# Kernel optimization log

Hardware: AMD Instinct MI355X
Metric: run time of the kernel (lower is better)

## Reference

```python
import jax, jax.numpy as jnp
import numpy as np
import math

B, SQ, SKV, D = 16, 1024, 1024, 256


def setup_inputs() -> dict:
    key = jax.random.key(0)
    kq, kk, kv, km = jax.random.split(key, 4)
    # Scale inputs down: the module applies exp() to raw QK^T logits, so dot
    # products must stay small to avoid overflow (std ~ 0.05^2*sqrt(D) ~ 0.04).
    scale = 0.05
    query = jax.random.normal(kq, (B, SQ, D), dtype=jnp.float32) * scale
    key_t = jax.random.normal(kk, (B, SKV, D), dtype=jnp.float32) * scale
    value = jax.random.normal(kv, (B, SKV, D), dtype=jnp.float32)
    mask = jax.random.randint(km, (B, SQ, SKV), 0, 2, dtype=jnp.int32)
    return {"query": query, "key": key_t, "value": value, "mask": mask}


def reference(query, key, value, mask):
    # scores = exp(Q K^T) / sqrt(d)  -- note: exp BEFORE scaling, as in source
    d = query.shape[-1]
    inv_sqrt_d = jnp.float32(1.0 / math.sqrt(d))
    scores = jnp.exp(jnp.einsum('bqd,bkd->bqk', query, key)) * inv_sqrt_d
    # masked_fill(mask == 0, -1e9)
    scores = jnp.where(mask == 0, jnp.float32(-1e9), scores)
    p_attn = jax.nn.softmax(scores, axis=-1)
    # dropout is identity in eval mode (deterministic reference)
    output = jnp.einsum('bqk,bkd->bqd', p_attn, value)
    # flatten=True path: sum over the query/sequence dim
    return output.sum(axis=1), p_attn
```

## Files before the change

### kernel.cpp

```cpp
#include <hip/hip_runtime.h>

#define NB   16
#define NSQ  1024
#define NSKV 1024
#define ND   256

typedef __bf16    bf16x8 __attribute__((ext_vector_type(8)));
typedef float     f32x4  __attribute__((ext_vector_type(4)));
typedef _Float16  f16x4  __attribute__((ext_vector_type(4)));

#define KST 264

__global__ __launch_bounds__(256) void cvt_k_bf16(
    const float* __restrict__ src, __bf16* __restrict__ dst)
{
    const int i = blockIdx.x * 256 + threadIdx.x;
    const float4* s = (const float4*)src + (size_t)i * 2;
    float4 a = s[0], b = s[1];
    bf16x8 o;
    o[0] = (__bf16)a.x; o[1] = (__bf16)a.y; o[2] = (__bf16)a.z; o[3] = (__bf16)a.w;
    o[4] = (__bf16)b.x; o[5] = (__bf16)b.y; o[6] = (__bf16)b.z; o[7] = (__bf16)b.w;
    ((bf16x8*)dst)[i] = o;
}

__global__ __launch_bounds__(256) void pack_mask(
    const int* __restrict__ mask, unsigned* __restrict__ mw)
{
    const int row = blockIdx.x * 4 + (threadIdx.x >> 6);
    const int l   = threadIdx.x & 63;
    const int4* mrow = (const int4*)(mask + (size_t)row * NSKV) + l * 4;
    unsigned w = 0;
    #pragma unroll
    for (int v = 0; v < 4; ++v) {
        int4 mv = mrow[v];
        w |= (mv.x != 0 ? 1u : 0u) << (v * 4 + 0);
        w |= (mv.y != 0 ? 1u : 0u) << (v * 4 + 1);
        w |= (mv.z != 0 ? 1u : 0u) << (v * 4 + 2);
        w |= (mv.w != 0 ? 1u : 0u) << (v * 4 + 3);
    }
    const int m    = l & 15;
    const int base = l & 48;
    unsigned out = 0;
    #pragma unroll
    for (int c = 0; c < 16; ++c) {
        unsigned v = (unsigned)__shfl((int)w, base | c);
        out |= ((v >> m) & 1u) << c;
    }
    mw[(size_t)row * 64 + l] = out;
}

__global__ __launch_bounds__(256, 2) void attn_fused(
    const float* __restrict__ Q, const __bf16* __restrict__ Kb,
    const unsigned* __restrict__ mw, float* __restrict__ out_p,
    float* __restrict__ colsum)
{
    const int b    = blockIdx.x >> 6;
    const int qt   = blockIdx.x & 63;
    const int q0   = qt * 16;
    const int tid  = threadIdx.x;
    const int lane = tid & 63;
    const int h    = tid >> 6;
    const int m    = lane & 15;
    const int kg   = lane >> 4;

    __shared__ __attribute__((aligned(16))) __bf16 kbuf[4][2][16 * KST];
    __shared__ float Zs[4][16];
    __shared__ float invZs[16];

    bf16x8 afrag[8];
    {
        const float* qbase = Q + ((size_t)(b * NSQ + q0 + m)) * ND;
        #pragma unroll
        for (int dc = 0; dc < 8; ++dc) {
            const float* p4 = qbase + dc * 32 + kg * 8;
            float4 x = *(const float4*)(p4);
            float4 y = *(const float4*)(p4 + 4);
            bf16x8 a;
            a[0] = (__bf16)x.x; a[1] = (__bf16)x.y; a[2] = (__bf16)x.z; a[3] = (__bf16)x.w;
            a[4] = (__bf16)y.x; a[5] = (__bf16)y.y; a[6] = (__bf16)y.z; a[7] = (__bf16)y.w;
            afrag[dc] = a;
        }
    }

    unsigned mword[4];
    #pragma unroll
    for (int i = 0; i < 4; ++i)
        mword[i] = mw[(size_t)(b * NSQ + q0 + kg * 4 + i) * 64 + h * 16 + m];

    const __bf16* kq   = Kb + ((size_t)(b * NSKV + h * 256)) * ND;
    const int     gcol = (lane & 31) * 8;
    const int     grow = lane >> 5;
    __bf16* buf0 = &kbuf[h][0][0];
    __bf16* buf1 = &kbuf[h][1][0];

    float zacc[4] = {0.f, 0.f, 0.f, 0.f};
    f16x4 ebuf[16];
    bf16x8 ga[8], gb[8];

    #define LDCHUNK(g, c) { \
        const __bf16* _p = kq + (size_t)(c) * 16 * ND + gcol; \
        _Pragma("unroll") \
        for (int r = 0; r < 8; ++r) \
            (g)[r] = *(const bf16x8*)(_p + (size_t)(2 * r + grow) * ND); }

    #define STCHUNK(g, buf) { \
        _Pragma("unroll") \
        for (int r = 0; r < 8; ++r) \
            *(bf16x8*)((buf) + (2 * r + grow) * KST + gcol) = (g)[r]; }

    #define COMPUTE(buf, c) { \
        f32x4 acc = {0.f, 0.f, 0.f, 0.f}; \
        _Pragma("unroll") \
        for (int dc = 0; dc < 8; ++dc) { \
            bf16x8 bfr = *(const bf16x8*)((buf) + m * KST + dc * 32 + kg * 8); \
            acc = __builtin_amdgcn_mfma_f32_16x16x32_bf16(afrag[dc], bfr, acc, 0, 0, 0); \
        } \
        _Pragma("unroll") \
        for (int i = 0; i < 4; ++i) { \
            float e = ((mword[i] >> (c)) & 1u) ? __expf(__expf(acc[i]) * 0.0625f) : 0.f; \
            zacc[i] += e; \
            ebuf[c][i] = (_Float16)e; \
        } }

    LDCHUNK(ga, 0);
    STCHUNK(ga, buf0);
    LDCHUNK(gb, 1);

    #pragma unroll
    for (int cc = 0; cc < 16; cc += 2) {
        COMPUTE(buf0, cc);
        STCHUNK(gb, buf1);
        if (cc + 2 < 16) LDCHUNK(ga, cc + 2);
        COMPUTE(buf1, cc + 1);
        if (cc + 2 < 16) STCHUNK(ga, buf0);
        if (cc + 3 < 16) LDCHUNK(gb, cc + 3);
    }

    _Float16* myE = (_Float16*)&kbuf[h][0][0];
    #pragma unroll
    for (int c = 0; c < 16; ++c)
        #pragma unroll
        for (int i = 0; i < 4; ++i)
            myE[(kg * 4 + i) * KST + c * 16 + m] = ebuf[c][i];

    #pragma unroll
    for (int i = 0; i < 4; ++i) {
        float z = zacc[i];
        z += __shfl_xor(z, 1);
        z += __shfl_xor(z, 2);
        z += __shfl_xor(z, 4);
        z += __shfl_xor(z, 8);
        if (m == 0) Zs[h][kg * 4 + i] = z;
    }
    __syncthreads();
    if (tid < 16)
        invZs[tid] = 1.0f / (Zs[0][tid] + Zs[1][tid] + Zs[2][tid] + Zs[3][tid]);
    __syncthreads();

    const size_t rowbase = (size_t)(b * NSQ + q0);
    float csum[4] = {0.f, 0.f, 0.f, 0.f};
    float* prow = out_p + rowbase * NSKV + h * 256 + lane * 4;
    #pragma unroll
    for (int s = 0; s < 16; ++s) {
        f16x4 ev = *(const f16x4*)&myE[s * KST + lane * 4];
        const float iz = invZs[s];
        float4 pv;
        pv.x = (float)ev[0] * iz; pv.y = (float)ev[1] * iz;
        pv.z = (float)ev[2] * iz; pv.w = (float)ev[3] * iz;
        *(float4*)(prow + (size_t)s * NSKV) = pv;
        csum[0] += pv.x; csum[1] += pv.y; csum[2] += pv.z; csum[3] += pv.w;
    }
    #pragma unroll
    for (int j = 0; j < 4; ++j)
        atomicAdd(&colsum[b * NSKV + h * 256 + lane * 4 + j], csum[j]);
}

__global__ __launch_bounds__(256) void attn_out_kernel(
    const float* __restrict__ colsum, const float* __restrict__ V,
    float* __restrict__ out)
{
    const int b  = blockIdx.x >> 6;
    const int ks = (blockIdx.x & 63) << 4;
    const int d  = threadIdx.x;
    float acc = 0.f;
    #pragma unroll
    for (int k = 0; k < 16; ++k) {
        acc += colsum[b * NSKV + ks + k] * V[((size_t)(b * NSKV + ks + k)) * ND + d];
    }
    atomicAdd(&out[b * ND + d], acc);
}

extern "C" void kernel_launch(void* const* d_in, const int* in_sizes, int n_in,
                              void* d_out, int out_size, void* d_ws, size_t ws_size,
                              hipStream_t stream)
{
    (void)in_sizes; (void)n_in; (void)out_size; (void)ws_size;
    const float* Q    = (const float*)d_in[0];
    const float* K    = (const float*)d_in[1];
    const float* V    = (const float*)d_in[2];
    const int*   mask = (const int*)d_in[3];

    float* out0 = (float*)d_out;
    float* p    = out0 + NB * ND;

    float*    colsum = (float*)d_ws;
    __bf16*   Kb     = (__bf16*)((char*)d_ws + (64 << 10));
    unsigned* mwbits = (unsigned*)((char*)d_ws + (64 << 10) + (size_t)NB * NSKV * ND * 2);

    hipMemsetAsync(colsum, 0, NB * NSKV * sizeof(float), stream);
    hipMemsetAsync(out0, 0, NB * ND * sizeof(float), stream);

    const int nK8 = NB * NSKV * ND / 8;
    cvt_k_bf16<<<nK8 / 256, 256, 0, stream>>>(K, Kb);
    pack_mask<<<NB * NSQ / 4, 256, 0, stream>>>(mask, mwbits);
    attn_fused<<<NB * 64, 256, 0, stream>>>(Q, Kb, mwbits, p, colsum);
    attn_out_kernel<<<NB * 64, 256, 0, stream>>>(colsum, V, out0);
}
```

Baseline: 208.4 us.

## Fuse K conversion, mask packing, attention and V reduction into one kernel

Replaces the four-kernel pipeline with a single kernel. Each block loads fp32 K and converts it to bf16 on the fly, stages raw int mask tiles in LDS, and computes the P·V column-sum product in its epilogue. The goal is to drop the separate conversion and packing passes, the colsum workspace and memset, and extra launches. In exchange, every block now re-reads fp32 K and the whole V slab for its batch, which duplicates heavy L2 traffic. It also adds a serial 1024-step loop per thread and raises register pressure from the fp32 staging buffers.

Result: slower. 337.6 us (+62.0%).

```diff
diff --git a/kernel.cpp b/kernel.cpp
--- a/kernel.cpp
+++ b/kernel.cpp
@@ -11,48 +11,10 @@
 
 #define KST 264
 
-__global__ __launch_bounds__(256) void cvt_k_bf16(
-    const float* __restrict__ src, __bf16* __restrict__ dst)
-{
-    const int i = blockIdx.x * 256 + threadIdx.x;
-    const float4* s = (const float4*)src + (size_t)i * 2;
-    float4 a = s[0], b = s[1];
-    bf16x8 o;
-    o[0] = (__bf16)a.x; o[1] = (__bf16)a.y; o[2] = (__bf16)a.z; o[3] = (__bf16)a.w;
-    o[4] = (__bf16)b.x; o[5] = (__bf16)b.y; o[6] = (__bf16)b.z; o[7] = (__bf16)b.w;
-    ((bf16x8*)dst)[i] = o;
-}
-
-__global__ __launch_bounds__(256) void pack_mask(
-    const int* __restrict__ mask, unsigned* __restrict__ mw)
-{
-    const int row = blockIdx.x * 4 + (threadIdx.x >> 6);
-    const int l   = threadIdx.x & 63;
-    const int4* mrow = (const int4*)(mask + (size_t)row * NSKV) + l * 4;
-    unsigned w = 0;
-    #pragma unroll
-    for (int v = 0; v < 4; ++v) {
-        int4 mv = mrow[v];
-        w |= (mv.x != 0 ? 1u : 0u) << (v * 4 + 0);
-        w |= (mv.y != 0 ? 1u : 0u) << (v * 4 + 1);
-        w |= (mv.z != 0 ? 1u : 0u) << (v * 4 + 2);
-        w |= (mv.w != 0 ? 1u : 0u) << (v * 4 + 3);
-    }
-    const int m    = l & 15;
-    const int base = l & 48;
-    unsigned out = 0;
-    #pragma unroll
-    for (int c = 0; c < 16; ++c) {
-        unsigned v = (unsigned)__shfl((int)w, base | c);
-        out |= ((v >> m) & 1u) << c;
-    }
-    mw[(size_t)row * 64 + l] = out;
-}
-
-__global__ __launch_bounds__(256, 2) void attn_fused(
-    const float* __restrict__ Q, const __bf16* __restrict__ Kb,
-    const unsigned* __restrict__ mw, float* __restrict__ out_p,
-    float* __restrict__ colsum)
+__global__ __launch_bounds__(256, 2) void attn_mega(
+    const float* __restrict__ Q, const float* __restrict__ K,
+    const float* __restrict__ V, const int* __restrict__ mask,
+    float* __restrict__ out0, float* __restrict__ out_p)
 {
     const int b    = blockIdx.x >> 6;
     const int qt   = blockIdx.x & 63;
@@ -64,6 +26,7 @@
     const int kg   = lane >> 4;
 
     __shared__ __attribute__((aligned(16))) __bf16 kbuf[4][2][16 * KST];
+    __shared__ __attribute__((aligned(16))) int    mbuf[4][2][256];
     __shared__ float Zs[4][16];
     __shared__ float invZs[16];
 
@@ -82,58 +45,63 @@
         }
     }
 
-    unsigned mword[4];
-    #pragma unroll
-    for (int i = 0; i < 4; ++i)
-        mword[i] = mw[(size_t)(b * NSQ + q0 + kg * 4 + i) * 64 + h * 16 + m];
+    const float* kq    = K + ((size_t)(b * NSKV + h * 256)) * ND;
+    const int*   maskB = mask + ((size_t)(b * NSQ + q0)) * NSKV + h * 256;
+    const int    grow  = lane >> 5;
+    const int    gcol  = (lane & 31) * 8;
+    const int    mrow  = lane >> 2;
+    const int    mcol  = (lane & 3) * 4;
 
-    const __bf16* kq   = Kb + ((size_t)(b * NSKV + h * 256)) * ND;
-    const int     gcol = (lane & 31) * 8;
-    const int     grow = lane >> 5;
-    __bf16* buf0 = &kbuf[h][0][0];
-    __bf16* buf1 = &kbuf[h][1][0];
+    float  zacc[4] = {0.f, 0.f, 0.f, 0.f};
+    f16x4  ebuf[16];
+    float4 ga[16];
+    int4   mreg;
 
-    float zacc[4] = {0.f, 0.f, 0.f, 0.f};
-    f16x4 ebuf[16];
-    bf16x8 ga[8], gb[8];
+    #define LDC(c) { \
+        const float* _p = kq + (size_t)(c) * 16 * ND + gcol; \
+        _Pragma("unroll") \
+        for (int r = 0; r < 8; ++r) { \
+            ga[2*r]   = *(const float4*)(_p + (size_t)(2*r + grow) * ND); \
+            ga[2*r+1] = *(const float4*)(_p + (size_t)(2*r + grow) * ND + 4); \
+        } \
+        mreg = *(const int4*)(maskB + (size_t)mrow * NSKV + (c) * 16 + mcol); }
 
-    #define LDCHUNK(g, c) { \
-        const __bf16* _p = kq + (size_t)(c) * 16 * ND + gcol; \
+    #define STC(pb) { \
+        __bf16* _b = &kbuf[h][pb][0]; \
         _Pragma("unroll") \
-        for (int r = 0; r < 8; ++r) \
-            (g)[r] = *(const bf16x8*)(_p + (size_t)(2 * r + grow) * ND); }
+        for (int r = 0; r < 8; ++r) { \
+            bf16x8 t; \
+            t[0]=(__bf16)ga[2*r].x;   t[1]=(__bf16)ga[2*r].y; \
+            t[2]=(__bf16)ga[2*r].z;   t[3]=(__bf16)ga[2*r].w; \
+            t[4]=(__bf16)ga[2*r+1].x; t[5]=(__bf16)ga[2*r+1].y; \
+            t[6]=(__bf16)ga[2*r+1].z; t[7]=(__bf16)ga[2*r+1].w; \
+            *(bf16x8*)(_b + (2*r + grow) * KST + gcol) = t; \
+        } \
+        *(int4*)&mbuf[h][pb][mrow * 16 + mcol] = mreg; }
 
-    #define STCHUNK(g, buf) { \
-        _Pragma("unroll") \
-        for (int r = 0; r < 8; ++r) \
-            *(bf16x8*)((buf) + (2 * r + grow) * KST + gcol) = (g)[r]; }
-
-    #define COMPUTE(buf, c) { \
+    #define CMP(c, pb) { \
+        const __bf16* _b = &kbuf[h][pb][0]; \
         f32x4 acc = {0.f, 0.f, 0.f, 0.f}; \
         _Pragma("unroll") \
         for (int dc = 0; dc < 8; ++dc) { \
-            bf16x8 bfr = *(const bf16x8*)((buf) + m * KST + dc * 32 + kg * 8); \
+            bf16x8 bfr = *(const bf16x8*)(_b + m * KST + dc * 32 + kg * 8); \
             acc = __builtin_amdgcn_mfma_f32_16x16x32_bf16(afrag[dc], bfr, acc, 0, 0, 0); \
         } \
         _Pragma("unroll") \
         for (int i = 0; i < 4; ++i) { \
-            float e = ((mword[i] >> (c)) & 1u) ? __expf(__expf(acc[i]) * 0.0625f) : 0.f; \
+            int mk = mbuf[h][pb][(kg * 4 + i) * 16 + m]; \
+            float e = mk ? __expf(__expf(acc[i]) * 0.0625f) : 0.f; \
             zacc[i] += e; \
             ebuf[c][i] = (_Float16)e; \
         } }
 
-    LDCHUNK(ga, 0);
-    STCHUNK(ga, buf0);
-    LDCHUNK(gb, 1);
-
+    LDC(0);
+    STC(0);
     #pragma unroll
-    for (int cc = 0; cc < 16; cc += 2) {
-        COMPUTE(buf0, cc);
-        STCHUNK(gb, buf1);
-        if (cc + 2 < 16) LDCHUNK(ga, cc + 2);
-        COMPUTE(buf1, cc + 1);
-        if (cc + 2 < 16) STCHUNK(ga, buf0);
-        if (cc + 3 < 16) LDCHUNK(gb, cc + 3);
+    for (int c = 0; c < 16; ++c) {
+        if (c < 15) LDC(c + 1);
+        CMP(c, c & 1);
+        if (c < 15) STC((c + 1) & 1);
     }
 
     _Float16* myE = (_Float16*)&kbuf[h][0][0];
@@ -157,9 +125,8 @@
         invZs[tid] = 1.0f / (Zs[0][tid] + Zs[1][tid] + Zs[2][tid] + Zs[3][tid]);
     __syncthreads();
 
-    const size_t rowbase = (size_t)(b * NSQ + q0);
     float csum[4] = {0.f, 0.f, 0.f, 0.f};
-    float* prow = out_p + rowbase * NSKV + h * 256 + lane * 4;
+    float* prow = out_p + (size_t)(b * NSQ + q0) * NSKV + h * 256 + lane * 4;
     #pragma unroll
     for (int s = 0; s < 16; ++s) {
         f16x4 ev = *(const f16x4*)&myE[s * KST + lane * 4];
@@ -170,31 +137,29 @@
         *(float4*)(prow + (size_t)s * NSKV) = pv;
         csum[0] += pv.x; csum[1] += pv.y; csum[2] += pv.z; csum[3] += pv.w;
     }
-    #pragma unroll
-    for (int j = 0; j < 4; ++j)
-        atomicAdd(&colsum[b * NSKV + h * 256 + lane * 4 + j], csum[j]);
-}
 
-__global__ __launch_bounds__(256) void attn_out_kernel(
-    const float* __restrict__ colsum, const float* __restrict__ V,
-    float* __restrict__ out)
-{
-    const int b  = blockIdx.x >> 6;
-    const int ks = (blockIdx.x & 63) << 4;
-    const int d  = threadIdx.x;
-    float acc = 0.f;
-    #pragma unroll
-    for (int k = 0; k < 16; ++k) {
-        acc += colsum[b * NSKV + ks + k] * V[((size_t)(b * NSKV + ks + k)) * ND + d];
-    }
-    atomicAdd(&out[b * ND + d], acc);
+    float* cs = (float*)&mbuf[0][0][0];
+    float4 fcs; fcs.x = csum[0]; fcs.y = csum[1]; fcs.z = csum[2]; fcs.w = csum[3];
+    *(float4*)&cs[h * 256 + lane * 4] = fcs;
+    __syncthreads();
+
+    const float* Vb = V + (size_t)b * NSKV * ND + tid;
+    float oacc = 0.f;
+    #pragma unroll 8
+    for (int k = 0; k < NSKV; ++k)
+        oacc += cs[k] * Vb[(size_t)k * ND];
+    atomicAdd(&out0[b * ND + tid], oacc);
+
+    #undef LDC
+    #undef STC
+    #undef CMP
 }
 
 extern "C" void kernel_launch(void* const* d_in, const int* in_sizes, int n_in,
                               void* d_out, int out_size, void* d_ws, size_t ws_size,
                               hipStream_t stream)
 {
-    (void)in_sizes; (void)n_in; (void)out_size; (void)ws_size;
+    (void)in_sizes; (void)n_in; (void)out_size; (void)d_ws; (void)ws_size;
     const float* Q    = (const float*)d_in[0];
     const float* K    = (const float*)d_in[1];
     const float* V    = (const float*)d_in[2];
@@ -203,16 +168,6 @@
     float* out0 = (float*)d_out;
     float* p    = out0 + NB * ND;
 
-    float*    colsum = (float*)d_ws;
-    __bf16*   Kb     = (__bf16*)((char*)d_ws + (64 << 10));
-    unsigned* mwbits = (unsigned*)((char*)d_ws + (64 << 10) + (size_t)NB * NSKV * ND * 2);
-
-    hipMemsetAsync(colsum, 0, NB * NSKV * sizeof(float), stream);
     hipMemsetAsync(out0, 0, NB * ND * sizeof(float), stream);
-
-    const int nK8 = NB * NSKV * ND / 8;
-    cvt_k_bf16<<<nK8 / 256, 256, 0, stream>>>(K, Kb);
-    pack_mask<<<NB * NSQ / 4, 256, 0, stream>>>(mask, mwbits);
-    attn_fused<<<NB * 64, 256, 0, stream>>>(Q, Kb, mwbits, p, colsum);
-    attn_out_kernel<<<NB * 64, 256, 0, stream>>>(colsum, V, out0);
+    attn_mega<<<NB * 64, 256, 0, stream>>>(Q, K, V, mask, out0, p);
 }
```

## Process 32 query rows per block to reuse each staged K tile twice

Applied to the files above, without the earlier changes.

Each block now handles two 16-row query tiles against the same K chunks. Every K tile staged in shared memory feeds two MFMA sequences, which halves K global loads and LDS staging per query row and halves the grid size. The K pipeline is restructured from two register buffers to a single register buffer with an alternating LDS slot, prefetching one chunk ahead. The cost is much higher register pressure (two Q fragment sets and two 16-entry exp buffers) and only 512 blocks, which may lower occupancy. The kernel is likely bound by writing the p_attn output, so the gain may be small.

Result: slower. 219.0 us (+5.1%).

```diff
diff --git a/kernel.cpp b/kernel.cpp
--- a/kernel.cpp
+++ b/kernel.cpp
@@ -54,9 +54,9 @@
     const unsigned* __restrict__ mw, float* __restrict__ out_p,
     float* __restrict__ colsum)
 {
-    const int b    = blockIdx.x >> 6;
-    const int qt   = blockIdx.x & 63;
-    const int q0   = qt * 16;
+    const int b    = blockIdx.x >> 5;
+    const int qt   = blockIdx.x & 31;
+    const int q0   = qt * 32;
     const int tid  = threadIdx.x;
     const int lane = tid & 63;
     const int h    = tid >> 6;
@@ -64,55 +64,64 @@
     const int kg   = lane >> 4;
 
     __shared__ __attribute__((aligned(16))) __bf16 kbuf[4][2][16 * KST];
-    __shared__ float Zs[4][16];
-    __shared__ float invZs[16];
-
-    bf16x8 afrag[8];
+    __shared__ float Zs[4][32];
+    __shared__ float invZs[32];
+
+    bf16x8 afragA[8], afragB[8];
     {
-        const float* qbase = Q + ((size_t)(b * NSQ + q0 + m)) * ND;
+        const float* qbaseA = Q + ((size_t)(b * NSQ + q0 + m)) * ND;
+        const float* qbaseB = qbaseA + 16 * ND;
         #pragma unroll
         for (int dc = 0; dc < 8; ++dc) {
-            const float* p4 = qbase + dc * 32 + kg * 8;
-            float4 x = *(const float4*)(p4);
-            float4 y = *(const float4*)(p4 + 4);
+            const int off = dc * 32 + kg * 8;
+            float4 x = *(const float4*)(qbaseA + off);
+            float4 y = *(const float4*)(qbaseA + off + 4);
             bf16x8 a;
             a[0] = (__bf16)x.x; a[1] = (__bf16)x.y; a[2] = (__bf16)x.z; a[3] = (__bf16)x.w;
             a[4] = (__bf16)y.x; a[5] = (__bf16)y.y; a[6] = (__bf16)y.z; a[7] = (__bf16)y.w;
-            afrag[dc] = a;
+            afragA[dc] = a;
+            x = *(const float4*)(qbaseB + off);
+            y = *(const float4*)(qbaseB + off + 4);
+            a[0] = (__bf16)x.x; a[1] = (__bf16)x.y; a[2] = (__bf16)x.z; a[3] = (__bf16)x.w;
+            a[4] = (__bf16)y.x; a[5] = (__bf16)y.y; a[6] = (__bf16)y.z; a[7] = (__bf16)y.w;
+            afragB[dc] = a;
         }
     }
 
-    unsigned mword[4];
-    #pragma unroll
-    for (int i = 0; i < 4; ++i)
-        mword[i] = mw[(size_t)(b * NSQ + q0 + kg * 4 + i) * 64 + h * 16 + m];
+    unsigned mwordA[4], mwordB[4];
+    #pragma unroll
+    for (int i = 0; i < 4; ++i) {
+        mwordA[i] = mw[(size_t)(b * NSQ + q0 + kg * 4 + i) * 64 + h * 16 + m];
+        mwordB[i] = mw[(size_t)(b * NSQ + q0 + 16 + kg * 4 + i) * 64 + h * 16 + m];
+    }
 
     const __bf16* kq   = Kb + ((size_t)(b * NSKV + h * 256)) * ND;
     const int     gcol = (lane & 31) * 8;
     const int     grow = lane >> 5;
-    __bf16* buf0 = &kbuf[h][0][0];
-    __bf16* buf1 = &kbuf[h][1][0];
-
-    float zacc[4] = {0.f, 0.f, 0.f, 0.f};
-    f16x4 ebuf[16];
-    bf16x8 ga[8], gb[8];
-
-    #define LDCHUNK(g, c) { \
+
+    float  zaccA[4] = {0.f, 0.f, 0.f, 0.f};
+    float  zaccB[4] = {0.f, 0.f, 0.f, 0.f};
+    f16x4  ebufA[16], ebufB[16];
+    bf16x8 ga[8];
+
+    #define LDC(c) { \
         const __bf16* _p = kq + (size_t)(c) * 16 * ND + gcol; \
         _Pragma("unroll") \
         for (int r = 0; r < 8; ++r) \
-            (g)[r] = *(const bf16x8*)(_p + (size_t)(2 * r + grow) * ND); }
-
-    #define STCHUNK(g, buf) { \
+            ga[r] = *(const bf16x8*)(_p + (size_t)(2 * r + grow) * ND); }
+
+    #define STC(pb) { \
+        __bf16* _b = &kbuf[h][pb][0]; \
         _Pragma("unroll") \
         for (int r = 0; r < 8; ++r) \
-            *(bf16x8*)((buf) + (2 * r + grow) * KST + gcol) = (g)[r]; }
-
-    #define COMPUTE(buf, c) { \
+            *(bf16x8*)(_b + (2 * r + grow) * KST + gcol) = ga[r]; }
+
+    #define CMP(afrag, ebuf, mword, zacc, c, pb) { \
+        const __bf16* _b = &kbuf[h][pb][0]; \
         f32x4 acc = {0.f, 0.f, 0.f, 0.f}; \
         _Pragma("unroll") \
         for (int dc = 0; dc < 8; ++dc) { \
-            bf16x8 bfr = *(const bf16x8*)((buf) + m * KST + dc * 32 + kg * 8); \
+            bf16x8 bfr = *(const bf16x8*)(_b + m * KST + dc * 32 + kg * 8); \
             acc = __builtin_amdgcn_mfma_f32_16x16x32_bf16(afrag[dc], bfr, acc, 0, 0, 0); \
         } \
         _Pragma("unroll") \
@@ -122,46 +131,46 @@
             ebuf[c][i] = (_Float16)e; \
         } }
 
-    LDCHUNK(ga, 0);
-    STCHUNK(ga, buf0);
-    LDCHUNK(gb, 1);
-
-    #pragma unroll
-    for (int cc = 0; cc < 16; cc += 2) {
-        COMPUTE(buf0, cc);
-        STCHUNK(gb, buf1);
-        if (cc + 2 < 16) LDCHUNK(ga, cc + 2);
-        COMPUTE(buf1, cc + 1);
-        if (cc + 2 < 16) STCHUNK(ga, buf0);
-        if (cc + 3 < 16) LDCHUNK(gb, cc + 3);
+    LDC(0);
+    STC(0);
+    #pragma unroll
+    for (int c = 0; c < 16; ++c) {
+        if (c < 15) LDC(c + 1);
+        CMP(afragA, ebufA, mwordA, zaccA, c, c & 1);
+        CMP(afragB, ebufB, mwordB, zaccB, c, c & 1);
+        if (c < 15) STC((c + 1) & 1);
     }
 
     _Float16* myE = (_Float16*)&kbuf[h][0][0];
     #pragma unroll
     for (int c = 0; c < 16; ++c)
         #pragma unroll
-        for (int i = 0; i < 4; ++i)
-            myE[(kg * 4 + i) * KST + c * 16 + m] = ebuf[c][i];
+        for (int i = 0; i < 4; ++i) {
+            myE[(kg * 4 + i) * KST + c * 16 + m]        = ebufA[c][i];
+            myE[(16 + kg * 4 + i) * KST + c * 16 + m]   = ebufB[c][i];
+        }
 
     #pragma unroll
     for (int i = 0; i < 4; ++i) {
-        float z = zacc[i];
-        z += __shfl_xor(z, 1);
-        z += __shfl_xor(z, 2);
-        z += __shfl_xor(z, 4);
-        z += __shfl_xor(z, 8);
-        if (m == 0) Zs[h][kg * 4 + i] = z;
+        float za = zaccA[i], zb = zaccB[i];
+        za += __shfl_xor(za, 1); zb += __shfl_xor(zb, 1);
+        za += __shfl_xor(za, 2); zb += __shfl_xor(zb, 2);
+        za += __shfl_xor(za, 4); zb += __shfl_xor(zb, 4);
+        za += __shfl_xor(za, 8); zb += __shfl_xor(zb, 8);
+        if (m == 0) {
+            Zs[h][kg * 4 + i]      = za;
+            Zs[h][16 + kg * 4 + i] = zb;
+        }
     }
     __syncthreads();
-    if (tid < 16)
+    if (tid < 32)
         invZs[tid] = 1.0f / (Zs[0][tid] + Zs[1][tid] + Zs[2][tid] + Zs[3][tid]);
     __syncthreads();
 
-    const size_t rowbase = (size_t)(b * NSQ + q0);
     float csum[4] = {0.f, 0.f, 0.f, 0.f};
-    float* prow = out_p + rowbase * NSKV + h * 256 + lane * 4;
-    #pragma unroll
-    for (int s = 0; s < 16; ++s) {
+    float* prow = out_p + (size_t)(b * NSQ + q0) * NSKV + h * 256 + lane * 4;
+    #pragma unroll
+    for (int s = 0; s < 32; ++s) {
         f16x4 ev = *(const f16x4*)&myE[s * KST + lane * 4];
         const float iz = invZs[s];
         float4 pv;
@@ -173,6 +182,10 @@
     #pragma unroll
     for (int j = 0; j < 4; ++j)
         atomicAdd(&colsum[b * NSKV + h * 256 + lane * 4 + j], csum[j]);
+
+    #undef LDC
+    #undef STC
+    #undef CMP
 }
 
 __global__ __launch_bounds__(256) void attn_out_kernel(
@@ -213,6 +226,6 @@
     const int nK8 = NB * NSKV * ND / 8;
     cvt_k_bf16<<<nK8 / 256, 256, 0, stream>>>(K, Kb);
     pack_mask<<<NB * NSQ / 4, 256, 0, stream>>>(mask, mwbits);
-    attn_fused<<<NB * 64, 256, 0, stream>>>(Q, Kb, mwbits, p, colsum);
+    attn_fused<<<NB * 32, 256, 0, stream>>>(Q, Kb, mwbits, p, colsum);
     attn_out_kernel<<<NB * 64, 256, 0, stream>>>(colsum, V, out0);
 }
```

## Merge prep kernels and memsets into one launch; issue K loads earlier

Applied to the files above, without the earlier changes.

Folds the K bf16 conversion, the mask bit-packing and the two zeroing memsets into a single prep kernel that dispatches on block index, cutting four launches down to one. It also reorders the double-buffered K-tile pipeline in the attention kernel so each global load is issued before the preceding MFMA compute rather than after it, giving the loads more time to hide latency. Issuing loads earlier keeps more registers live and may raise register pressure.

New measurement: 201.8 us. 1.03x faster.

```diff
diff --git a/kernel.cpp b/kernel.cpp
--- a/kernel.cpp
+++ b/kernel.cpp
@@ -11,42 +11,48 @@
 
 #define KST 264
 
-__global__ __launch_bounds__(256) void cvt_k_bf16(
-    const float* __restrict__ src, __bf16* __restrict__ dst)
-{
-    const int i = blockIdx.x * 256 + threadIdx.x;
-    const float4* s = (const float4*)src + (size_t)i * 2;
-    float4 a = s[0], b = s[1];
-    bf16x8 o;
-    o[0] = (__bf16)a.x; o[1] = (__bf16)a.y; o[2] = (__bf16)a.z; o[3] = (__bf16)a.w;
-    o[4] = (__bf16)b.x; o[5] = (__bf16)b.y; o[6] = (__bf16)b.z; o[7] = (__bf16)b.w;
-    ((bf16x8*)dst)[i] = o;
-}
-
-__global__ __launch_bounds__(256) void pack_mask(
-    const int* __restrict__ mask, unsigned* __restrict__ mw)
-{
-    const int row = blockIdx.x * 4 + (threadIdx.x >> 6);
-    const int l   = threadIdx.x & 63;
-    const int4* mrow = (const int4*)(mask + (size_t)row * NSKV) + l * 4;
-    unsigned w = 0;
-    #pragma unroll
-    for (int v = 0; v < 4; ++v) {
-        int4 mv = mrow[v];
-        w |= (mv.x != 0 ? 1u : 0u) << (v * 4 + 0);
-        w |= (mv.y != 0 ? 1u : 0u) << (v * 4 + 1);
-        w |= (mv.z != 0 ? 1u : 0u) << (v * 4 + 2);
-        w |= (mv.w != 0 ? 1u : 0u) << (v * 4 + 3);
-    }
-    const int m    = l & 15;
-    const int base = l & 48;
-    unsigned out = 0;
-    #pragma unroll
-    for (int c = 0; c < 16; ++c) {
-        unsigned v = (unsigned)__shfl((int)w, base | c);
-        out |= ((v >> m) & 1u) << c;
-    }
-    mw[(size_t)row * 64 + l] = out;
+__global__ __launch_bounds__(256) void prep_kernel(
+    const float* __restrict__ K, __bf16* __restrict__ Kb,
+    const int* __restrict__ mask, unsigned* __restrict__ mw,
+    float* __restrict__ colsum, float* __restrict__ out0)
+{
+    const int bid = blockIdx.x;
+    const int tid = threadIdx.x;
+    if (bid < 2048) {
+        const int i = bid * 256 + tid;
+        const float4* s = (const float4*)K + (size_t)i * 2;
+        float4 a = s[0], b = s[1];
+        bf16x8 o;
+        o[0] = (__bf16)a.x; o[1] = (__bf16)a.y; o[2] = (__bf16)a.z; o[3] = (__bf16)a.w;
+        o[4] = (__bf16)b.x; o[5] = (__bf16)b.y; o[6] = (__bf16)b.z; o[7] = (__bf16)b.w;
+        ((bf16x8*)Kb)[i] = o;
+    } else if (bid < 2048 + 4096) {
+        const int row = (bid - 2048) * 4 + (tid >> 6);
+        const int l   = tid & 63;
+        const int4* mrow = (const int4*)(mask + (size_t)row * NSKV) + l * 4;
+        unsigned w = 0;
+        #pragma unroll
+        for (int v = 0; v < 4; ++v) {
+            int4 mv = mrow[v];
+            w |= (mv.x != 0 ? 1u : 0u) << (v * 4 + 0);
+            w |= (mv.y != 0 ? 1u : 0u) << (v * 4 + 1);
+            w |= (mv.z != 0 ? 1u : 0u) << (v * 4 + 2);
+            w |= (mv.w != 0 ? 1u : 0u) << (v * 4 + 3);
+        }
+        const int m    = l & 15;
+        const int base = l & 48;
+        unsigned out = 0;
+        #pragma unroll
+        for (int c = 0; c < 16; ++c) {
+            unsigned v = (unsigned)__shfl((int)w, base | c);
+            out |= ((v >> m) & 1u) << c;
+        }
+        mw[(size_t)row * 64 + l] = out;
+    } else if (bid < 2048 + 4096 + 64) {
+        colsum[(bid - 6144) * 256 + tid] = 0.f;
+    } else {
+        out0[(bid - 6208) * 256 + tid] = 0.f;
+    }
 }
 
 __global__ __launch_bounds__(256, 2) void attn_fused(
@@ -93,8 +99,8 @@
     __bf16* buf0 = &kbuf[h][0][0];
     __bf16* buf1 = &kbuf[h][1][0];
 
-    float zacc[4] = {0.f, 0.f, 0.f, 0.f};
-    f16x4 ebuf[16];
+    float  zacc[4] = {0.f, 0.f, 0.f, 0.f};
+    f16x4  ebuf[16];
     bf16x8 ga[8], gb[8];
 
     #define LDCHUNK(g, c) { \
@@ -123,17 +129,17 @@
         } }
 
     LDCHUNK(ga, 0);
+    LDCHUNK(gb, 1);
     STCHUNK(ga, buf0);
-    LDCHUNK(gb, 1);
 
     #pragma unroll
     for (int cc = 0; cc < 16; cc += 2) {
+        if (cc + 2 < 16) LDCHUNK(ga, cc + 2);
         COMPUTE(buf0, cc);
         STCHUNK(gb, buf1);
-        if (cc + 2 < 16) LDCHUNK(ga, cc + 2);
+        if (cc + 3 < 16) LDCHUNK(gb, cc + 3);
         COMPUTE(buf1, cc + 1);
         if (cc + 2 < 16) STCHUNK(ga, buf0);
-        if (cc + 3 < 16) LDCHUNK(gb, cc + 3);
     }
 
     _Float16* myE = (_Float16*)&kbuf[h][0][0];
@@ -157,9 +163,8 @@
         invZs[tid] = 1.0f / (Zs[0][tid] + Zs[1][tid] + Zs[2][tid] + Zs[3][tid]);
     __syncthreads();
 
-    const size_t rowbase = (size_t)(b * NSQ + q0);
     float csum[4] = {0.f, 0.f, 0.f, 0.f};
-    float* prow = out_p + rowbase * NSKV + h * 256 + lane * 4;
+    float* prow = out_p + (size_t)(b * NSQ + q0) * NSKV + h * 256 + lane * 4;
     #pragma unroll
     for (int s = 0; s < 16; ++s) {
         f16x4 ev = *(const f16x4*)&myE[s * KST + lane * 4];
@@ -173,6 +178,10 @@
     #pragma unroll
     for (int j = 0; j < 4; ++j)
         atomicAdd(&colsum[b * NSKV + h * 256 + lane * 4 + j], csum[j]);
+
+    #undef LDCHUNK
+    #undef STCHUNK
+    #undef COMPUTE
 }
 
 __global__ __launch_bounds__(256) void attn_out_kernel(
@@ -207,12 +216,7 @@
     __bf16*   Kb     = (__bf16*)((char*)d_ws + (64 << 10));
     unsigned* mwbits = (unsigned*)((char*)d_ws + (64 << 10) + (size_t)NB * NSKV * ND * 2);
 
-    hipMemsetAsync(colsum, 0, NB * NSKV * sizeof(float), stream);
-    hipMemsetAsync(out0, 0, NB * ND * sizeof(float), stream);
-
-    const int nK8 = NB * NSKV * ND / 8;
-    cvt_k_bf16<<<nK8 / 256, 256, 0, stream>>>(K, Kb);
-    pack_mask<<<NB * NSQ / 4, 256, 0, stream>>>(mask, mwbits);
+    prep_kernel<<<6224, 256, 0, stream>>>(K, Kb, mask, mwbits, colsum, out0);
     attn_fused<<<NB * 64, 256, 0, stream>>>(Q, Kb, mwbits, p, colsum);
     attn_out_kernel<<<NB * 64, 256, 0, stream>>>(colsum, V, out0);
 }
```
